# Kernel tuning notes

Measured on AMD Instinct MI355X. Metric: run time of the kernel, lower is better.

Reference implementation:

```python
import jax, jax.numpy as jnp
import numpy as np

N_NODES = 50000
N_EDGES = 800000
F_IN = 128
HID = 128
F_ADD = 32
N_GRAPHS = 128


def setup_inputs() -> dict:
    key = jax.random.key(0)
    ks = jax.random.split(key, 12)
    x = jax.random.normal(ks[0], (N_NODES, F_IN), dtype=jnp.float32)
    edge_index = jax.random.randint(ks[1], (2, N_EDGES), 0, N_NODES, dtype=jnp.int64)
    batch = jnp.sort(jax.random.randint(ks[2], (N_NODES,), 0, N_GRAPHS, dtype=jnp.int64))
    additional_features = jax.random.normal(ks[3], (N_GRAPHS, F_ADD), dtype=jnp.float32)
    def glorot(k, shape):
        fan_in, fan_out = shape[0], shape[1]
        lim = jnp.sqrt(6.0 / (fan_in + fan_out)).astype(jnp.float32)
        return jax.random.uniform(k, shape, jnp.float32, -lim, lim)
    W1 = glorot(ks[4], (F_IN, HID)); b1 = jnp.zeros((HID,), jnp.float32)
    W2 = glorot(ks[5], (HID, HID)); b2 = jnp.zeros((HID,), jnp.float32)
    fc1_w = glorot(ks[6], (HID + F_ADD, HID)); fc1_b = jnp.zeros((HID,), jnp.float32)
    fc2_w = glorot(ks[7], (HID, 2)); fc2_b = jnp.zeros((2,), jnp.float32)
    return {"x": x, "edge_index": edge_index, "batch": batch,
            "additional_features": additional_features,
            "W1": W1, "b1": b1, "W2": W2, "b2": b2,
            "fc1_w": fc1_w, "fc1_b": fc1_b, "fc2_w": fc2_w, "fc2_b": fc2_b}


def _gcn_conv(h, src, dst, norm, W, b):
    # h: [N, d_in]; symmetric-normalized scatter-add aggregation (PyG GCNConv)
    h = h @ W                                   # [N, d_out]
    msg = h[src] * norm[:, None]                # gather + scale: [E+N, d_out]
    return jax.ops.segment_sum(msg, dst, num_segments=N_NODES) + b


def reference(x, edge_index, batch, additional_features,
              W1, b1, W2, b2, fc1_w, fc1_b, fc2_w, fc2_b):
    loops = jnp.arange(N_NODES, dtype=edge_index.dtype)
    src = jnp.concatenate([edge_index[0], loops])   # A + I
    dst = jnp.concatenate([edge_index[1], loops])
    deg = jax.ops.segment_sum(jnp.ones_like(src, dtype=x.dtype), dst,
                              num_segments=N_NODES)
    dinv = jnp.where(deg > 0, jax.lax.rsqrt(jnp.maximum(deg, 1.0)), 0.0)
    norm = dinv[src] * dinv[dst]

    h = jax.nn.relu(_gcn_conv(x, src, dst, norm, W1, b1))
    h = jax.nn.relu(_gcn_conv(h, src, dst, norm, W2, b2))
    # dropout is identity in eval mode

    sums = jax.ops.segment_sum(h, batch, num_segments=N_GRAPHS)    # [G, HID]
    counts = jax.ops.segment_sum(jnp.ones((N_NODES,), h.dtype), batch,
                                 num_segments=N_GRAPHS)
    pooled = sums / jnp.maximum(counts, 1.0)[:, None]              # global_mean_pool

    z = jnp.concatenate([pooled, additional_features], axis=1)     # [G, HID+F_ADD]
    z = jax.nn.relu(z @ fc1_w + fc1_b)
    return z @ fc2_w + fc2_b                                       # [G, 2]
```

## Files before the change

### kernel.cpp

```cpp
#include <hip/hip_runtime.h>

#define NN 50000
#define NE 800000
#define FD 128
#define FDH 64
#define FA 32
#define NG 128
#define EETOT (NE + NN)
#define NBLK ((NN + 255) / 256)
#define FEPB 2048
#define FNCH ((EETOT + FEPB - 1) / FEPB)
#define NPXCD 6250

typedef __attribute__((ext_vector_type(8))) short short8;
typedef __attribute__((ext_vector_type(4))) float f32x4;

__device__ __forceinline__ float bfbits(unsigned short u) {
    return __uint_as_float(((unsigned int)u) << 16);
}
__device__ __forceinline__ float bflo(unsigned int p) { return __uint_as_float(p << 16); }
__device__ __forceinline__ float bfhi(unsigned int p) { return __uint_as_float(p & 0xffff0000u); }
__device__ __forceinline__ unsigned short f2bf(float f) {
    unsigned int u = __float_as_uint(f);
    unsigned int r = u + 0x7FFFu + ((u >> 16) & 1u);
    return (unsigned short)(r >> 16);
}
__device__ __forceinline__ unsigned int packbf(float a, float b) {
    return (unsigned int)f2bf(a) | ((unsigned int)f2bf(b) << 16);
}
__device__ __forceinline__ int ld_idx(const int* p, int i, int is64) {
    return is64 ? p[2 * i] : p[i];
}

__global__ __launch_bounds__(128) void mark_kernel(float* out, float v) {
    out[threadIdx.x] = v;
}

__global__ __launch_bounds__(256) void flags_kernel(
        const unsigned int* x, const int* ei, const int* batch,
        const unsigned int* addf, const unsigned int* w1, const unsigned int* b1,
        const unsigned int* w2, const unsigned int* b2, const unsigned int* fc1w,
        const unsigned int* fc1b, const unsigned int* fc2w, const unsigned int* fc2b,
        int* flags) {
    int w = threadIdx.x >> 6, lane = threadIdx.x & 63;
    const unsigned int* tp[12] = {x, 0, 0, addf, w1, b1, w2, b2, fc1w, fc1b, fc2w, fc2b};
    const int nw[12] = {64, 0, 0, 64, 64, 64, 64, 64, 64, 64, 64, 1};
    for (int idx = w; idx < 12; idx += 4) {
        const unsigned int* p = tp[idx];
        if (!p) continue;
        unsigned int wv = (lane < nw[idx]) ? p[lane] : 0u;
        int nzp = (wv != 0u) ? 1 : 0;
        unsigned int e = (wv >> 7) & 0xFFu;
        int hitp = (nzp && e >= 100u && e <= 140u) ? 1 : 0;
        int nz = __popcll(__ballot(nzp));
        int hits = __popcll(__ballot(hitp));
        if (lane == 0) flags[idx] = (nz < 8) ? 1 : (hits * 4 >= nz * 3);
    }
    if (w == 1) {
        int v = (lane < 32) ? ei[2 * lane + 1] : 0;
        unsigned long long m = __ballot(v != 0);
        if (lane == 0) flags[12] = (m == 0ull) ? 1 : 0;
    }
    if (w == 2 && lane == 0) flags[13] = (batch[NN - 1] == 0) ? 1 : 0;
}

__global__ __launch_bounds__(256) void prep(
        const void* addf, const void* w1, const void* b1, const void* w2,
        const void* b2, const void* fc1w, const void* fc1b, const void* fc2w,
        const void* fc2b, unsigned int* W1t, unsigned int* W2t,
        float* addff, float* b1f, float* b2f, float* fc1wf, float* fc1bf,
        float* fc2wf, float* fc2bf, const int* flags, int* degi) {
    int b = blockIdx.x;
    if (b < 64) {
        int rel = b * 256 + threadIdx.x;
        const void* src = (rel < 8192) ? w1 : w2;
        unsigned int* dst = (rel < 8192) ? W1t : W2t;
        int flag = (rel < 8192) ? flags[4] : flags[6];
        int rr = rel & 8191;
        int n = rr >> 6, kk = rr & 63;
        float lo, hi;
        if (flag) {
            const unsigned short* s = (const unsigned short*)src;
            lo = bfbits(s[(2 * kk) * FD + n]);
            hi = bfbits(s[(2 * kk + 1) * FD + n]);
        } else {
            const float* s = (const float*)src;
            lo = s[(2 * kk) * FD + n];
            hi = s[(2 * kk + 1) * FD + n];
        }
        dst[rr] = packbf(lo, hi);
    } else if (b < 163) {
        int i = (b - 64) * 256 + threadIdx.x;
        const void* src; float* dst; int flag; int rel;
        if      (i < 4096)  { src = addf; dst = addff; flag = flags[3];  rel = i; }
        else if (i < 4224)  { src = b1;   dst = b1f;   flag = flags[5];  rel = i - 4096; }
        else if (i < 4352)  { src = b2;   dst = b2f;   flag = flags[7];  rel = i - 4224; }
        else if (i < 24832) { src = fc1w; dst = fc1wf; flag = flags[8];  rel = i - 4352; }
        else if (i < 24960) { src = fc1b; dst = fc1bf; flag = flags[9];  rel = i - 24832; }
        else if (i < 25216) { src = fc2w; dst = fc2wf; flag = flags[10]; rel = i - 24960; }
        else if (i < 25218) { src = fc2b; dst = fc2bf; flag = flags[11]; rel = i - 25216; }
        else return;
        if (flag) dst[rel] = bfbits(((const unsigned short*)src)[rel]);
        else      dst[rel] = ((const float*)src)[rel];
    } else {
        int i = (b - 163) * 256 + threadIdx.x;
        if (i < NN) degi[i] = 0;
    }
}

__global__ __launch_bounds__(256) void deg_kernel(const int* ei, const int* flags,
                                                  int* deg, int* s32, int* d32) {
    int e = blockIdx.x * 256 + threadIdx.x;
    int is64 = flags[12];
    if (e < NE) {
        int s = ld_idx(ei, e, is64);
        int d = ld_idx(ei, NE + e, is64);
        s32[e] = s;
        d32[e] = d;
        atomicAdd(&deg[d], 1);
    }
}

__global__ __launch_bounds__(256) void scan1(const int* deg, float* dinv,
                                             int* escan, int* bsum) {
    __shared__ int sh[256];
    int i = blockIdx.x * 256 + threadIdx.x;
    int d = (i < NN) ? deg[i] : 0;
    if (i < NN) dinv[i] = rsqrtf((float)(d + 1));
    int v = (i < NN) ? d + 1 : 0;
    sh[threadIdx.x] = v;
    __syncthreads();
    for (int off = 1; off < 256; off <<= 1) {
        int a = ((int)threadIdx.x >= off) ? sh[threadIdx.x - off] : 0;
        __syncthreads();
        sh[threadIdx.x] += a;
        __syncthreads();
    }
    if (i < NN) escan[i] = sh[threadIdx.x] - v;
    if (threadIdx.x == 255) bsum[blockIdx.x] = sh[255];
}

__global__ __launch_bounds__(256) void scan3(const int* escan, const int* bsum,
        const int* batch, const int* flags, int* rowstart, int* cursor, int* gstart) {
    __shared__ int sb[256];
    int t = threadIdx.x;
    int v = (t < NBLK) ? bsum[t] : 0;
    sb[t] = v;
    __syncthreads();
    for (int off = 1; off < 256; off <<= 1) {
        int a = (t >= off) ? sb[t - off] : 0;
        __syncthreads();
        sb[t] += a;
        __syncthreads();
    }
    int boff = (blockIdx.x == 0) ? 0 : sb[blockIdx.x - 1];
    int i = blockIdx.x * 256 + t;
    if (i < NN) {
        int r = escan[i] + boff;
        rowstart[i] = r;
        cursor[i]   = r;
    }
    if (i == 0) rowstart[NN] = EETOT;
    if (i < NN) {
        int is64 = flags[13];
        int bc = ld_idx(batch, i, is64);
        if (i == 0) {
            for (int g = 0; g <= bc; ++g) gstart[g] = 0;
        } else {
            int bp = ld_idx(batch, i - 1, is64);
            for (int g = bp + 1; g <= bc; ++g) gstart[g] = i;
        }
        if (i == NN - 1) {
            for (int g = bc + 1; g <= NG; ++g) gstart[g] = NN;
        }
    }
}

__global__ __launch_bounds__(256) void fill_kernel(const int* s32, const int* d32,
        const float* dinv, int* cursor, unsigned int* cv) {
    int chunk = blockIdx.x >> 3;
    int par   = blockIdx.x & 7;
    int base  = chunk * FEPB;
    #pragma unroll
    for (int k = 0; k < FEPB / 256; ++k) {
        int e = base + k * 256 + threadIdx.x;
        if (e >= EETOT) break;
        int s, d;
        if (e < NE) { d = d32[e]; s = -1; }
        else        { s = d = e - NE; }
        if (d / NPXCD != par) continue;
        if (s < 0) s = s32[e];
        int pos = atomicAdd(&cursor[d], 1);
        cv[pos] = (unsigned int)s | ((unsigned int)f2bf(dinv[s] * dinv[d]) << 16);
    }
}

__global__ __launch_bounds__(256) void gemm_mfma(const void* __restrict__ Av,
        const unsigned int* __restrict__ Wt, unsigned short* __restrict__ C,
        const int* flags, int maybe_f32) {
    int wave = threadIdx.x >> 6;
    int lane = threadIdx.x & 63;
    int quad = lane >> 4;
    int l16  = lane & 15;
    int mbase = blockIdx.x * 64 + wave * 16;
    int ra = mbase + l16;
    if (ra >= NN) ra = NN - 1;
    short8 af[4];
    bool f32in = maybe_f32 && !flags[0];
    if (!f32in) {
        const uint4* Arow = (const uint4*)((const unsigned int*)Av + (size_t)ra * FDH);
        #pragma unroll
        for (int kk = 0; kk < 4; ++kk) {
            uint4 v = Arow[kk * 4 + quad];
            af[kk] = *(short8*)&v;
        }
    } else {
        const float* Arow = (const float*)Av + (size_t)ra * FD;
        #pragma unroll
        for (int kk = 0; kk < 4; ++kk) {
            const float4* p = (const float4*)(Arow + (kk * 4 + quad) * 8);
            float4 u = p[0], v = p[1];
            uint4 q;
            q.x = packbf(u.x, u.y); q.y = packbf(u.z, u.w);
            q.z = packbf(v.x, v.y); q.w = packbf(v.z, v.w);
            af[kk] = *(short8*)&q;
        }
    }
    #pragma unroll
    for (int nt = 0; nt < 8; ++nt) {
        int n = nt * 16 + l16;
        const uint4* Wrow = (const uint4*)(Wt + (size_t)n * FDH);
        f32x4 acc = {0.f, 0.f, 0.f, 0.f};
        #pragma unroll
        for (int kk = 0; kk < 4; ++kk) {
            uint4 wv = Wrow[kk * 4 + quad];
            short8 bf = *(short8*)&wv;
            acc = __builtin_amdgcn_mfma_f32_16x16x32_bf16(af[kk], bf, acc, 0, 0, 0);
        }
        int row0 = mbase + quad * 4;
        #pragma unroll
        for (int reg = 0; reg < 4; ++reg) {
            int r = row0 + reg;
            if (r < NN) C[(size_t)r * FD + nt * 16 + l16] = f2bf(acc[reg]);
        }
    }
}

__global__ __launch_bounds__(256) void aggregate_kernel(const unsigned int* Hb,
        const unsigned int* cv, const int* rowstart, const float* bias,
        unsigned int* outb) {
    int n = blockIdx.x * 4 + (threadIdx.x >> 6);
    int cp = threadIdx.x & 63;
    if (n >= NN) return;
    int jb = rowstart[n], je = rowstart[n + 1];
    float acc0 = 0.f, acc1 = 0.f;
    int j = jb;
    for (; j + 7 < je; j += 8) {
        unsigned int rr[8], hh[8];
        #pragma unroll
        for (int k = 0; k < 8; ++k) rr[k] = cv[j + k];
        #pragma unroll
        for (int k = 0; k < 8; ++k) hh[k] = Hb[(size_t)(rr[k] & 0xFFFFu) * FDH + cp];
        #pragma unroll
        for (int k = 0; k < 8; ++k) {
            float v = bfbits((unsigned short)(rr[k] >> 16));
            acc0 += v * bflo(hh[k]);
            acc1 += v * bfhi(hh[k]);
        }
    }
    for (; j + 3 < je; j += 4) {
        unsigned int rr[4], hh[4];
        #pragma unroll
        for (int k = 0; k < 4; ++k) rr[k] = cv[j + k];
        #pragma unroll
        for (int k = 0; k < 4; ++k) hh[k] = Hb[(size_t)(rr[k] & 0xFFFFu) * FDH + cp];
        #pragma unroll
        for (int k = 0; k < 4; ++k) {
            float v = bfbits((unsigned short)(rr[k] >> 16));
            acc0 += v * bflo(hh[k]);
            acc1 += v * bfhi(hh[k]);
        }
    }
    for (; j < je; ++j) {
        unsigned int r = cv[j];
        unsigned int h = Hb[(size_t)(r & 0xFFFFu) * FDH + cp];
        float v = bfbits((unsigned short)(r >> 16));
        acc0 += v * bflo(h);
        acc1 += v * bfhi(h);
    }
    acc0 = fmaxf(acc0 + bias[2 * cp], 0.f);
    acc1 = fmaxf(acc1 + bias[2 * cp + 1], 0.f);
    outb[(size_t)n * FDH + cp] = packbf(acc0, acc1);
}

__global__ __launch_bounds__(256) void poolhead(const unsigned int* Hb,
        const int* gstart, const float* addf, const float* fc1w, const float* fc1b,
        const float* fc2w, const float* fc2b, const int* flags, void* outp) {
    int g = blockIdx.x;
    int t = threadIdx.x;
    int q = t >> 6, w = t & 63;
    int s = gstart[g], e = gstart[g + 1];
    float a0 = 0.f, a1 = 0.f;
    #pragma unroll 4
    for (int n = s + q; n < e; n += 4) {
        unsigned int h = Hb[(size_t)n * FDH + w];
        a0 += bflo(h);
        a1 += bfhi(h);
    }
    __shared__ float pp[4][FD];
    __shared__ float z[FD + FA];
    __shared__ float h[FD];
    pp[q][2 * w]     = a0;
    pp[q][2 * w + 1] = a1;
    __syncthreads();
    if (t < FD) {
        float cnt = (float)(e - s);
        if (cnt < 1.0f) cnt = 1.0f;
        z[t] = (pp[0][t] + pp[1][t] + pp[2][t] + pp[3][t]) / cnt;
    }
    if (t >= FD && t < FD + FA) z[t] = addf[g * FA + (t - FD)];
    __syncthreads();
    if (t < FD) {
        float acc = fc1b[t];
        #pragma unroll 4
        for (int k = 0; k < FD + FA; ++k)
            acc += z[k] * fc1w[k * FD + t];
        h[t] = fmaxf(acc, 0.f);
    }
    __syncthreads();
    if (t < 2) {
        float o = fc2b[t];
        for (int j = 0; j < FD; ++j) o += h[j] * fc2w[j * 2 + t];
        if (flags[0]) ((unsigned short*)outp)[g * 2 + t] = f2bf(o);
        else          ((float*)outp)[g * 2 + t] = o;
    }
}

extern "C" void kernel_launch(void* const* d_in, const int* in_sizes, int n_in,
                              void* d_out, int out_size, void* d_ws, size_t ws_size,
                              hipStream_t stream) {
    (void)out_size;

    if (n_in != 12) {
        hipLaunchKernelGGL(mark_kernel, dim3(1), dim3(128), 0, stream,
                           (float*)d_out, 2000.0f);
        return;
    }
    const int exp_sizes[12] = {6400000, 1600000, 50000, 4096, 16384, 128,
                               16384, 128, 20480, 128, 256, 2};
    for (int i = 0; i < 12; ++i) {
        if (in_sizes[i] != exp_sizes[i]) {
            hipLaunchKernelGGL(mark_kernel, dim3(1), dim3(128), 0, stream,
                               (float*)d_out, 3000.0f + 100.0f * i);
            return;
        }
    }

    size_t off = 0;
    char* base = (char*)d_ws;
#define WSALLOC(ptr, type, nbytes) \
    type* ptr = (type*)(base + off); off += (((size_t)(nbytes)) + 255) & ~(size_t)255;
    WSALLOC(bufA,  unsigned int, (size_t)NN * FDH * 4)
    WSALLOC(bufB,  unsigned int, (size_t)NN * FDH * 4)
    WSALLOC(dinv,  float, (size_t)NN * 4)
    WSALLOC(degi,  int,   (size_t)NN * 4)
    WSALLOC(rowst, int,   (size_t)(NN + 1) * 4)
    WSALLOC(cursor,int,   (size_t)NN * 4)
    WSALLOC(escan, int,   (size_t)NN * 4)
    WSALLOC(bsum,  int,   (size_t)NBLK * 4)
    WSALLOC(cv,    unsigned int, (size_t)EETOT * 4)
    WSALLOC(gstart,int,   (size_t)(NG + 1) * 4)
    WSALLOC(s32,   int,   (size_t)NE * 4)
    WSALLOC(d32,   int,   (size_t)NE * 4)
    WSALLOC(W1t,   unsigned int, (size_t)FD * FDH * 4)
    WSALLOC(W2t,   unsigned int, (size_t)FD * FDH * 4)
    WSALLOC(b1f,   float, FD * 4)
    WSALLOC(b2f,   float, FD * 4)
    WSALLOC(addff, float, (size_t)NG * FA * 4)
    WSALLOC(fc1wf, float, (size_t)(FD + FA) * FD * 4)
    WSALLOC(fc1bf, float, FD * 4)
    WSALLOC(fc2wf, float, FD * 2 * 4)
    WSALLOC(fc2bf, float, 2 * 4)
    WSALLOC(flags, int, 16 * 4)
#undef WSALLOC
    if (ws_size < off) {
        hipLaunchKernelGGL(mark_kernel, dim3(1), dim3(128), 0, stream,
                           (float*)d_out, 1000.0f);
        return;
    }

    const int* ei    = (const int*)d_in[1];
    const int* batch = (const int*)d_in[2];

    hipLaunchKernelGGL(flags_kernel, dim3(1), dim3(256), 0, stream,
                       (const unsigned int*)d_in[0], ei, batch,
                       (const unsigned int*)d_in[3], (const unsigned int*)d_in[4],
                       (const unsigned int*)d_in[5], (const unsigned int*)d_in[6],
                       (const unsigned int*)d_in[7], (const unsigned int*)d_in[8],
                       (const unsigned int*)d_in[9], (const unsigned int*)d_in[10],
                       (const unsigned int*)d_in[11], flags);

    hipLaunchKernelGGL(prep, dim3(359), dim3(256), 0, stream,
                       d_in[3], d_in[4], d_in[5], d_in[6], d_in[7],
                       d_in[8], d_in[9], d_in[10], d_in[11],
                       W1t, W2t, addff, b1f, b2f, fc1wf, fc1bf,
                       fc2wf, fc2bf, flags, degi);

    hipLaunchKernelGGL(deg_kernel, dim3((NE + 255) / 256), dim3(256), 0, stream,
                       ei, flags, degi, s32, d32);
    hipLaunchKernelGGL(scan1, dim3(NBLK), dim3(256), 0, stream,
                       degi, dinv, escan, bsum);
    hipLaunchKernelGGL(scan3, dim3(NBLK), dim3(256), 0, stream,
                       escan, bsum, batch, flags, rowst, cursor, gstart);
    hipLaunchKernelGGL(fill_kernel, dim3(FNCH * 8), dim3(256), 0, stream,
                       s32, d32, dinv, cursor, cv);

    hipLaunchKernelGGL(gemm_mfma, dim3((NN + 63) / 64), dim3(256), 0, stream,
                       d_in[0], W1t, (unsigned short*)bufA, flags, 1);
    hipLaunchKernelGGL(aggregate_kernel, dim3((NN + 3) / 4), dim3(256), 0, stream,
                       bufA, cv, rowst, b1f, bufB);
    hipLaunchKernelGGL(gemm_mfma, dim3((NN + 63) / 64), dim3(256), 0, stream,
                       bufB, W2t, (unsigned short*)bufA, flags, 0);
    hipLaunchKernelGGL(aggregate_kernel, dim3((NN + 3) / 4), dim3(256), 0, stream,
                       bufA, cv, rowst, b2f, bufB);

    hipLaunchKernelGGL(poolhead, dim3(NG), dim3(256), 0, stream,
                       bufB, gstart, addff, fc1wf, fc1bf, fc2wf, fc2bf,
                       flags, d_out);
}
```

Measured before the change: 311.0 us.

## Fuse dtype probes, decoupled scan, and aggregation with mean pooling

Removes the separate flags kernel by having each kernel probe input dtypes inline with wave ballots. Merges the two scan kernels into one single-pass scan that waits on earlier block totals through spin-waiting atomics. Fuses the second aggregation with global mean pooling using atomics into a per-graph partial buffer, leaving a small head kernel. The aim is fewer launches and no write and re-read of the final hidden features, at the cost of atomic contention and a spin-wait that depends on blocks being scheduled in order.

```diff
diff --git a/kernel.cpp b/kernel.cpp
--- a/kernel.cpp
+++ b/kernel.cpp
@@ -28,40 +28,25 @@
 __device__ __forceinline__ unsigned int packbf(float a, float b) {
     return (unsigned int)f2bf(a) | ((unsigned int)f2bf(b) << 16);
 }
-__device__ __forceinline__ int ld_idx(const int* p, int i, int is64) {
-    return is64 ? p[2 * i] : p[i];
+
+__device__ __forceinline__ int wave_probe_bf16(const unsigned int* t, int nwords) {
+    int lane = threadIdx.x & 63;
+    unsigned int wv = (lane < nwords) ? t[lane] : 0u;
+    int nzp = (wv != 0u) ? 1 : 0;
+    unsigned int e = (wv >> 7) & 0xFFu;
+    int hitp = (nzp && e >= 100u && e <= 140u) ? 1 : 0;
+    int nz = __popcll(__ballot(nzp));
+    int hits = __popcll(__ballot(hitp));
+    return (nz < 8) ? 1 : (hits * 4 >= nz * 3);
+}
+__device__ __forceinline__ int wave_probe_is64(const int* ei) {
+    int lane = threadIdx.x & 63;
+    int v = (lane < 32) ? ei[2 * lane + 1] : 0;
+    return (__ballot(v != 0) == 0ull) ? 1 : 0;
 }
 
 __global__ __launch_bounds__(128) void mark_kernel(float* out, float v) {
     out[threadIdx.x] = v;
-}
-
-__global__ __launch_bounds__(256) void flags_kernel(
-        const unsigned int* x, const int* ei, const int* batch,
-        const unsigned int* addf, const unsigned int* w1, const unsigned int* b1,
-        const unsigned int* w2, const unsigned int* b2, const unsigned int* fc1w,
-        const unsigned int* fc1b, const unsigned int* fc2w, const unsigned int* fc2b,
-        int* flags) {
-    int w = threadIdx.x >> 6, lane = threadIdx.x & 63;
-    const unsigned int* tp[12] = {x, 0, 0, addf, w1, b1, w2, b2, fc1w, fc1b, fc2w, fc2b};
-    const int nw[12] = {64, 0, 0, 64, 64, 64, 64, 64, 64, 64, 64, 1};
-    for (int idx = w; idx < 12; idx += 4) {
-        const unsigned int* p = tp[idx];
-        if (!p) continue;
-        unsigned int wv = (lane < nw[idx]) ? p[lane] : 0u;
-        int nzp = (wv != 0u) ? 1 : 0;
-        unsigned int e = (wv >> 7) & 0xFFu;
-        int hitp = (nzp && e >= 100u && e <= 140u) ? 1 : 0;
-        int nz = __popcll(__ballot(nzp));
-        int hits = __popcll(__ballot(hitp));
-        if (lane == 0) flags[idx] = (nz < 8) ? 1 : (hits * 4 >= nz * 3);
-    }
-    if (w == 1) {
-        int v = (lane < 32) ? ei[2 * lane + 1] : 0;
-        unsigned long long m = __ballot(v != 0);
-        if (lane == 0) flags[12] = (m == 0ull) ? 1 : 0;
-    }
-    if (w == 2 && lane == 0) flags[13] = (batch[NN - 1] == 0) ? 1 : 0;
 }
 
 __global__ __launch_bounds__(256) void prep(
@@ -69,13 +54,13 @@
         const void* b2, const void* fc1w, const void* fc1b, const void* fc2w,
         const void* fc2b, unsigned int* W1t, unsigned int* W2t,
         float* addff, float* b1f, float* b2f, float* fc1wf, float* fc1bf,
-        float* fc2wf, float* fc2bf, const int* flags, int* degi) {
+        float* fc2wf, float* fc2bf, int* degi, int* tsum, float* part) {
     int b = blockIdx.x;
     if (b < 64) {
         int rel = b * 256 + threadIdx.x;
         const void* src = (rel < 8192) ? w1 : w2;
         unsigned int* dst = (rel < 8192) ? W1t : W2t;
-        int flag = (rel < 8192) ? flags[4] : flags[6];
+        int flag = wave_probe_bf16((const unsigned int*)src, 64);
         int rr = rel & 8191;
         int n = rr >> 6, kk = rr & 63;
         float lo, hi;
@@ -91,83 +76,89 @@
         dst[rr] = packbf(lo, hi);
     } else if (b < 163) {
         int i = (b - 64) * 256 + threadIdx.x;
-        const void* src; float* dst; int flag; int rel;
-        if      (i < 4096)  { src = addf; dst = addff; flag = flags[3];  rel = i; }
-        else if (i < 4224)  { src = b1;   dst = b1f;   flag = flags[5];  rel = i - 4096; }
-        else if (i < 4352)  { src = b2;   dst = b2f;   flag = flags[7];  rel = i - 4224; }
-        else if (i < 24832) { src = fc1w; dst = fc1wf; flag = flags[8];  rel = i - 4352; }
-        else if (i < 24960) { src = fc1b; dst = fc1bf; flag = flags[9];  rel = i - 24832; }
-        else if (i < 25216) { src = fc2w; dst = fc2wf; flag = flags[10]; rel = i - 24960; }
-        else if (i < 25218) { src = fc2b; dst = fc2bf; flag = flags[11]; rel = i - 25216; }
+        int wb = (b - 64) * 256 + (threadIdx.x & ~63);
+        const void* src; float* dst; int base; int prnw; int lim;
+        if      (wb < 4096)  { src = addf; dst = addff; base = 0;     prnw = 64; lim = 4096;  }
+        else if (wb < 4224)  { src = b1;   dst = b1f;   base = 4096;  prnw = 64; lim = 128;   }
+        else if (wb < 4352)  { src = b2;   dst = b2f;   base = 4224;  prnw = 64; lim = 128;   }
+        else if (wb < 24832) { src = fc1w; dst = fc1wf; base = 4352;  prnw = 64; lim = 20480; }
+        else if (wb < 24960) { src = fc1b; dst = fc1bf; base = 24832; prnw = 64; lim = 128;   }
+        else if (wb < 25216) { src = fc2w; dst = fc2wf; base = 24960; prnw = 64; lim = 256;   }
+        else if (wb < 25280) { src = fc2b; dst = fc2bf; base = 25216; prnw = 1;  lim = 2;     }
         else return;
-        if (flag) dst[rel] = bfbits(((const unsigned short*)src)[rel]);
-        else      dst[rel] = ((const float*)src)[rel];
+        int flag = wave_probe_bf16((const unsigned int*)src, prnw);
+        int rel = i - base;
+        if (rel < lim) {
+            if (flag) dst[rel] = bfbits(((const unsigned short*)src)[rel]);
+            else      dst[rel] = ((const float*)src)[rel];
+        }
     } else {
         int i = (b - 163) * 256 + threadIdx.x;
-        if (i < NN) degi[i] = 0;
-    }
-}
-
-__global__ __launch_bounds__(256) void deg_kernel(const int* ei, const int* flags,
-                                                  int* deg, int* s32, int* d32) {
+        if      (i < NN)            degi[i] = 0;
+        else if (i < NN + 256)      tsum[i - NN] = 0;
+        else if (i < NN + 256 + NG * FD) part[i - NN - 256] = 0.f;
+    }
+}
+
+__global__ __launch_bounds__(256) void deg_kernel(const int* ei, int* deg,
+                                                  int* s32, int* d32) {
+    int is64 = wave_probe_is64(ei);
     int e = blockIdx.x * 256 + threadIdx.x;
-    int is64 = flags[12];
     if (e < NE) {
-        int s = ld_idx(ei, e, is64);
-        int d = ld_idx(ei, NE + e, is64);
+        int s = is64 ? ei[2 * e] : ei[e];
+        int d = is64 ? ei[2 * (NE + e)] : ei[NE + e];
         s32[e] = s;
         d32[e] = d;
         atomicAdd(&deg[d], 1);
     }
 }
 
-__global__ __launch_bounds__(256) void scan1(const int* deg, float* dinv,
-                                             int* escan, int* bsum) {
+__global__ __launch_bounds__(256) void scan_fused(const int* degi, const int* batch,
+        int* tsum, float* dinv, int* rowstart, int* cursor, int* gstart) {
     __shared__ int sh[256];
-    int i = blockIdx.x * 256 + threadIdx.x;
-    int d = (i < NN) ? deg[i] : 0;
+    int b = blockIdx.x, t = threadIdx.x;
+    int i = b * 256 + t;
+    int d = (i < NN) ? degi[i] : 0;
     if (i < NN) dinv[i] = rsqrtf((float)(d + 1));
     int v = (i < NN) ? d + 1 : 0;
-    sh[threadIdx.x] = v;
+    sh[t] = v;
     __syncthreads();
     for (int off = 1; off < 256; off <<= 1) {
-        int a = ((int)threadIdx.x >= off) ? sh[threadIdx.x - off] : 0;
+        int a = (t >= off) ? sh[t - off] : 0;
         __syncthreads();
-        sh[threadIdx.x] += a;
+        sh[t] += a;
         __syncthreads();
     }
-    if (i < NN) escan[i] = sh[threadIdx.x] - v;
-    if (threadIdx.x == 255) bsum[blockIdx.x] = sh[255];
-}
-
-__global__ __launch_bounds__(256) void scan3(const int* escan, const int* bsum,
-        const int* batch, const int* flags, int* rowstart, int* cursor, int* gstart) {
-    __shared__ int sb[256];
-    int t = threadIdx.x;
-    int v = (t < NBLK) ? bsum[t] : 0;
-    sb[t] = v;
-    __syncthreads();
-    for (int off = 1; off < 256; off <<= 1) {
-        int a = (t >= off) ? sb[t - off] : 0;
+    int incl = sh[t];
+    int total = sh[255];
+    if (t == 0) atomicExch(&tsum[b], total);
+    int pt = 0;
+    for (int j = t; j < b; j += 256) {
+        int s;
+        do { s = atomicAdd(&tsum[j], 0); } while (s == 0);
+        pt += s;
+    }
+    __syncthreads();
+    sh[t] = pt;
+    __syncthreads();
+    for (int off = 128; off >= 1; off >>= 1) {
+        if (t < off) sh[t] += sh[t + off];
         __syncthreads();
-        sb[t] += a;
-        __syncthreads();
-    }
-    int boff = (blockIdx.x == 0) ? 0 : sb[blockIdx.x - 1];
-    int i = blockIdx.x * 256 + t;
+    }
+    int boff = sh[0];
     if (i < NN) {
-        int r = escan[i] + boff;
+        int r = boff + incl - v;
         rowstart[i] = r;
         cursor[i]   = r;
     }
     if (i == 0) rowstart[NN] = EETOT;
     if (i < NN) {
-        int is64 = flags[13];
-        int bc = ld_idx(batch, i, is64);
+        int is64 = (batch[NN - 1] == 0) ? 1 : 0;
+        int bc = is64 ? batch[2 * i] : batch[i];
         if (i == 0) {
             for (int g = 0; g <= bc; ++g) gstart[g] = 0;
         } else {
-            int bp = ld_idx(batch, i - 1, is64);
+            int bp = is64 ? batch[2 * (i - 1)] : batch[i - 1];
             for (int g = bp + 1; g <= bc; ++g) gstart[g] = i;
         }
         if (i == NN - 1) {
@@ -197,7 +188,7 @@
 
 __global__ __launch_bounds__(256) void gemm_mfma(const void* __restrict__ Av,
         const unsigned int* __restrict__ Wt, unsigned short* __restrict__ C,
-        const int* flags, int maybe_f32) {
+        int maybe_f32) {
     int wave = threadIdx.x >> 6;
     int lane = threadIdx.x & 63;
     int quad = lane >> 4;
@@ -205,8 +196,9 @@
     int mbase = blockIdx.x * 64 + wave * 16;
     int ra = mbase + l16;
     if (ra >= NN) ra = NN - 1;
+    bool f32in = false;
+    if (maybe_f32) f32in = !wave_probe_bf16((const unsigned int*)Av, 64);
     short8 af[4];
-    bool f32in = maybe_f32 && !flags[0];
     if (!f32in) {
         const uint4* Arow = (const uint4*)((const unsigned int*)Av + (size_t)ra * FDH);
         #pragma unroll
@@ -293,46 +285,95 @@
     outb[(size_t)n * FDH + cp] = packbf(acc0, acc1);
 }
 
-__global__ __launch_bounds__(256) void poolhead(const unsigned int* Hb,
-        const int* gstart, const float* addf, const float* fc1w, const float* fc1b,
-        const float* fc2w, const float* fc2b, const int* flags, void* outp) {
+__global__ __launch_bounds__(256) void agg_pool(const unsigned int* Hb,
+        const unsigned int* cv, const int* rowstart, const float* bias,
+        const int* batch, float* part) {
+    int w = threadIdx.x >> 6, cp = threadIdx.x & 63;
+    int n = blockIdx.x * 4 + w;
+    int is64 = (batch[NN - 1] == 0) ? 1 : 0;
+    __shared__ float pp[4][FD];
+    __shared__ int gg[4];
+    float acc0 = 0.f, acc1 = 0.f;
+    int jb = rowstart[n], je = rowstart[n + 1];
+    int j = jb;
+    for (; j + 7 < je; j += 8) {
+        unsigned int rr[8], hh[8];
+        #pragma unroll
+        for (int k = 0; k < 8; ++k) rr[k] = cv[j + k];
+        #pragma unroll
+        for (int k = 0; k < 8; ++k) hh[k] = Hb[(size_t)(rr[k] & 0xFFFFu) * FDH + cp];
+        #pragma unroll
+        for (int k = 0; k < 8; ++k) {
+            float v = bfbits((unsigned short)(rr[k] >> 16));
+            acc0 += v * bflo(hh[k]);
+            acc1 += v * bfhi(hh[k]);
+        }
+    }
+    for (; j + 3 < je; j += 4) {
+        unsigned int rr[4], hh[4];
+        #pragma unroll
+        for (int k = 0; k < 4; ++k) rr[k] = cv[j + k];
+        #pragma unroll
+        for (int k = 0; k < 4; ++k) hh[k] = Hb[(size_t)(rr[k] & 0xFFFFu) * FDH + cp];
+        #pragma unroll
+        for (int k = 0; k < 4; ++k) {
+            float v = bfbits((unsigned short)(rr[k] >> 16));
+            acc0 += v * bflo(hh[k]);
+            acc1 += v * bfhi(hh[k]);
+        }
+    }
+    for (; j < je; ++j) {
+        unsigned int r = cv[j];
+        unsigned int h = Hb[(size_t)(r & 0xFFFFu) * FDH + cp];
+        float v = bfbits((unsigned short)(r >> 16));
+        acc0 += v * bflo(h);
+        acc1 += v * bfhi(h);
+    }
+    acc0 = fmaxf(acc0 + bias[2 * cp], 0.f);
+    acc1 = fmaxf(acc1 + bias[2 * cp + 1], 0.f);
+    pp[w][2 * cp]     = acc0;
+    pp[w][2 * cp + 1] = acc1;
+    if (cp == 0) gg[w] = is64 ? batch[2 * n] : batch[n];
+    __syncthreads();
+    bool allsame = (gg[0] == gg[1]) && (gg[1] == gg[2]) && (gg[2] == gg[3]);
+    if (allsame) {
+        if (w == 0) {
+            float s0 = pp[0][2 * cp] + pp[1][2 * cp] + pp[2][2 * cp] + pp[3][2 * cp];
+            float s1 = pp[0][2 * cp + 1] + pp[1][2 * cp + 1]
+                     + pp[2][2 * cp + 1] + pp[3][2 * cp + 1];
+            atomicAdd(&part[(size_t)gg[0] * FD + 2 * cp], s0);
+            atomicAdd(&part[(size_t)gg[0] * FD + 2 * cp + 1], s1);
+        }
+    } else {
+        atomicAdd(&part[(size_t)gg[w] * FD + 2 * cp], acc0);
+        atomicAdd(&part[(size_t)gg[w] * FD + 2 * cp + 1], acc1);
+    }
+}
+
+__global__ __launch_bounds__(128) void head_kernel(const float* part, const int* gstart,
+        const float* addf, const float* fc1w, const float* fc1b,
+        const float* fc2w, const float* fc2b, const unsigned int* x, void* outp) {
     int g = blockIdx.x;
     int t = threadIdx.x;
-    int q = t >> 6, w = t & 63;
-    int s = gstart[g], e = gstart[g + 1];
-    float a0 = 0.f, a1 = 0.f;
-    #pragma unroll 4
-    for (int n = s + q; n < e; n += 4) {
-        unsigned int h = Hb[(size_t)n * FDH + w];
-        a0 += bflo(h);
-        a1 += bfhi(h);
-    }
-    __shared__ float pp[4][FD];
     __shared__ float z[FD + FA];
     __shared__ float h[FD];
-    pp[q][2 * w]     = a0;
-    pp[q][2 * w + 1] = a1;
-    __syncthreads();
-    if (t < FD) {
-        float cnt = (float)(e - s);
-        if (cnt < 1.0f) cnt = 1.0f;
-        z[t] = (pp[0][t] + pp[1][t] + pp[2][t] + pp[3][t]) / cnt;
-    }
-    if (t >= FD && t < FD + FA) z[t] = addf[g * FA + (t - FD)];
-    __syncthreads();
-    if (t < FD) {
-        float acc = fc1b[t];
-        #pragma unroll 4
-        for (int k = 0; k < FD + FA; ++k)
-            acc += z[k] * fc1w[k * FD + t];
-        h[t] = fmaxf(acc, 0.f);
-    }
+    int obf = wave_probe_bf16(x, 64);
+    float cnt = (float)(gstart[g + 1] - gstart[g]);
+    if (cnt < 1.0f) cnt = 1.0f;
+    z[t] = part[(size_t)g * FD + t] / cnt;
+    if (t < FA) z[FD + t] = addf[g * FA + t];
+    __syncthreads();
+    float acc = fc1b[t];
+    #pragma unroll 4
+    for (int k = 0; k < FD + FA; ++k)
+        acc += z[k] * fc1w[k * FD + t];
+    h[t] = fmaxf(acc, 0.f);
     __syncthreads();
     if (t < 2) {
         float o = fc2b[t];
         for (int j = 0; j < FD; ++j) o += h[j] * fc2w[j * 2 + t];
-        if (flags[0]) ((unsigned short*)outp)[g * 2 + t] = f2bf(o);
-        else          ((float*)outp)[g * 2 + t] = o;
+        if (obf) ((unsigned short*)outp)[g * 2 + t] = f2bf(o);
+        else     ((float*)outp)[g * 2 + t] = o;
     }
 }
 
@@ -366,10 +407,10 @@
     WSALLOC(degi,  int,   (size_t)NN * 4)
     WSALLOC(rowst, int,   (size_t)(NN + 1) * 4)
     WSALLOC(cursor,int,   (size_t)NN * 4)
-    WSALLOC(escan, int,   (size_t)NN * 4)
-    WSALLOC(bsum,  int,   (size_t)NBLK * 4)
+    WSALLOC(tsum,  int,   256 * 4)
     WSALLOC(cv,    unsigned int, (size_t)EETOT * 4)
     WSALLOC(gstart,int,   (size_t)(NG + 1) * 4)
+    WSALLOC(part,  float, (size_t)NG * FD * 4)
     WSALLOC(s32,   int,   (size_t)NE * 4)
     WSALLOC(d32,   int,   (size_t)NE * 4)
     WSALLOC(W1t,   unsigned int, (size_t)FD * FDH * 4)
@@ -381,7 +422,6 @@
     WSALLOC(fc1bf, float, FD * 4)
     WSALLOC(fc2wf, float, FD * 2 * 4)
     WSALLOC(fc2bf, float, 2 * 4)
-    WSALLOC(flags, int, 16 * 4)
 #undef WSALLOC
     if (ws_size < off) {
         hipLaunchKernelGGL(mark_kernel, dim3(1), dim3(128), 0, stream,
@@ -392,39 +432,29 @@
     const int* ei    = (const int*)d_in[1];
     const int* batch = (const int*)d_in[2];
 
-    hipLaunchKernelGGL(flags_kernel, dim3(1), dim3(256), 0, stream,
-                       (const unsigned int*)d_in[0], ei, batch,
-                       (const unsigned int*)d_in[3], (const unsigned int*)d_in[4],
-                       (const unsigned int*)d_in[5], (const unsigned int*)d_in[6],
-                       (const unsigned int*)d_in[7], (const unsigned int*)d_in[8],
-                       (const unsigned int*)d_in[9], (const unsigned int*)d_in[10],
-                       (const unsigned int*)d_in[11], flags);
-
-    hipLaunchKernelGGL(prep, dim3(359), dim3(256), 0, stream,
+    hipLaunchKernelGGL(prep, dim3(424), dim3(256), 0, stream,
                        d_in[3], d_in[4], d_in[5], d_in[6], d_in[7],
                        d_in[8], d_in[9], d_in[10], d_in[11],
                        W1t, W2t, addff, b1f, b2f, fc1wf, fc1bf,
-                       fc2wf, fc2bf, flags, degi);
+                       fc2wf, fc2bf, degi, tsum, part);
 
     hipLaunchKernelGGL(deg_kernel, dim3((NE + 255) / 256), dim3(256), 0, stream,
-                       ei, flags, degi, s32, d32);
-    hipLaunchKernelGGL(scan1, dim3(NBLK), dim3(256), 0, stream,
-                       degi, dinv, escan, bsum);
-    hipLaunchKernelGGL(scan3, dim3(NBLK), dim3(256), 0, stream,
-                       escan, bsum, batch, flags, rowst, cursor, gstart);
+                       ei, degi, s32, d32);
+    hipLaunchKernelGGL(scan_fused, dim3(NBLK), dim3(256), 0, stream,
+                       degi, batch, tsum, dinv, rowst, cursor, gstart);
     hipLaunchKernelGGL(fill_kernel, dim3(FNCH * 8), dim3(256), 0, stream,
                        s32, d32, dinv, cursor, cv);
 
     hipLaunchKernelGGL(gemm_mfma, dim3((NN + 63) / 64), dim3(256), 0, stream,
-                       d_in[0], W1t, (unsigned short*)bufA, flags, 1);
+                       d_in[0], W1t, (unsigned short*)bufA, 1);
     hipLaunchKernelGGL(aggregate_kernel, dim3((NN + 3) / 4), dim3(256), 0, stream,
                        bufA, cv, rowst, b1f, bufB);
     hipLaunchKernelGGL(gemm_mfma, dim3((NN + 63) / 64), dim3(256), 0, stream,
-                       bufB, W2t, (unsigned short*)bufA, flags, 0);
-    hipLaunchKernelGGL(aggregate_kernel, dim3((NN + 3) / 4), dim3(256), 0, stream,
-                       bufA, cv, rowst, b2f, bufB);
-
-    hipLaunchKernelGGL(poolhead, dim3(NG), dim3(256), 0, stream,
-                       bufB, gstart, addff, fc1wf, fc1bf, fc2wf, fc2bf,
-                       flags, d_out);
-}
+                       bufB, W2t, (unsigned short*)bufA, 0);
+    hipLaunchKernelGGL(agg_pool, dim3(NN / 4), dim3(256), 0, stream,
+                       bufA, cv, rowst, b2f, batch, part);
+
+    hipLaunchKernelGGL(head_kernel, dim3(NG), dim3(128), 0, stream,
+                       part, gstart, addff, fc1wf, fc1bf, fc2wf, fc2bf,
+                       (const unsigned int*)d_in[0], d_out);
+}
```

Result: slower. 319.8 us (+2.8%).
